# Kernel tuning notes

Measured on AMD Instinct MI355X. Metric: run time of the kernel, lower is better.

## Reference

```python
import jax, jax.numpy as jnp
import numpy as np

DIM = 1024
HEADS = 16
HEAD_DIM = DIM // HEADS  # 64


def get_rope_matrix(seq_len: int, dim: int) -> jnp.ndarray:
    # rope[s, d] = concat(cos(s * inv_freq), sin(s * inv_freq))  -> (seq_len, dim)
    half = dim // 2
    inv_freq = 1.0 / (10000.0 ** (jnp.arange(half, dtype=jnp.float32) / half))
    sinusoid = jnp.arange(seq_len, dtype=jnp.float32)[:, None] * inv_freq[None, :]
    return jnp.concatenate([jnp.cos(sinusoid), jnp.sin(sinusoid)], axis=-1)


def setup_inputs() -> dict:
    key = jax.random.key(0)
    ks = jax.random.split(key, 6)
    B, T, D = 2, 2048, DIM
    scale = 1.0 / np.sqrt(D)
    return {
        "x": jax.random.normal(ks[0], (B, T, D), dtype=jnp.float32),
        "Wq": jax.random.normal(ks[1], (D, D), dtype=jnp.float32) * scale,
        "Wk": jax.random.normal(ks[2], (D, D), dtype=jnp.float32) * scale,
        "Wv": jax.random.normal(ks[3], (D, D), dtype=jnp.float32) * scale,
        "Wo": jax.random.normal(ks[4], (D, D), dtype=jnp.float32) * scale,
        "bo": jax.random.normal(ks[5], (D,), dtype=jnp.float32) * 0.01,
    }


def reference(x, Wq, Wk, Wv, Wo, bo):
    B, T, D = x.shape
    H, hd = HEADS, HEAD_DIM

    # projections -> (B, H, T, hd)
    def split_heads(y):
        return y.reshape(B, T, H, hd).transpose(0, 2, 1, 3)

    q = split_heads(x @ Wq)
    k = split_heads(x @ Wk)
    v = split_heads(x @ Wv)

    rope = get_rope_matrix(T, hd)  # (T, hd)

    # apply_rope(v, rope): einsum('...nd,sd->...ns') contracts head_dim -> (B,H,T,T)
    v_r = jnp.einsum('bhnd,sd->bhns', v, rope)

    scores = jax.nn.softmax(jnp.einsum('bhnd,bhmd->bhnm', q, k) / jnp.sqrt(jnp.float32(hd)), axis=-1)
    out = jnp.einsum('bhnm,bhms->bhns', scores, v_r)  # (B,H,T,T)

    # apply_rope(out, rope.T): out2[...,n,s] = sum_t out[...,n,t] * rope[t,s] -> (B,H,T,hd)
    out = jnp.einsum('bhnt,ts->bhns', out, rope)

    out = out.transpose(0, 2, 1, 3).reshape(B, T, D)
    return out @ Wo + bo
```

## Files before the change

kernel.cpp:

```cpp
#include <hip/hip_runtime.h>
#include <math.h>

#define DIM 1024
#define NH 16
#define HD 64
#define TT 2048
#define NTOK 4096

typedef __bf16 bf8v __attribute__((ext_vector_type(8)));
typedef float f4v __attribute__((ext_vector_type(4)));
typedef float f16v __attribute__((ext_vector_type(16)));
typedef unsigned short us8 __attribute__((ext_vector_type(8)));
typedef unsigned short us4 __attribute__((ext_vector_type(4)));
typedef unsigned int u4v __attribute__((ext_vector_type(4)));

static __device__ __forceinline__ unsigned short f2bf(float f) {
    unsigned int u = __float_as_uint(f);
    u += 0x7FFFu + ((u >> 16) & 1u);
    return (unsigned short)(u >> 16);
}
static __device__ __forceinline__ bf8v ld8(const unsigned short* p) {
    return __builtin_bit_cast(bf8v, *(const us8*)p);
}
static __device__ __forceinline__ void gl_lds(const unsigned short* g, unsigned short* l) {
    __builtin_amdgcn_global_load_lds((const __attribute__((address_space(1))) unsigned int*)(g),
                                     (__attribute__((address_space(3))) unsigned int*)(l), 16, 0, 0);
}

__global__ void k_prep(const float* __restrict__ x, unsigned short* __restrict__ xb,
                       const float* __restrict__ Wq, const float* __restrict__ Wk,
                       const float* __restrict__ Wv, unsigned short* __restrict__ wt,
                       float* __restrict__ rope) {
    int tid = threadIdx.x;
    int bb = blockIdx.x;
    if (bb < 4096) {
        int i = bb * 256 + tid;
        float4 v = ((const float4*)x)[i];
        us4 o;
        o[0] = f2bf(v.x); o[1] = f2bf(v.y); o[2] = f2bf(v.z); o[3] = f2bf(v.w);
        *(us4*)&xb[i * 4] = o;
    } else if (bb < 7168) {
        __shared__ float tile[32][33];
        bb -= 4096;
        int z = bb >> 10, rem = bb & 1023;
        int bx = rem & 31, by = rem >> 5;
        const float* W = (z == 0) ? Wq : ((z == 1) ? Wk : Wv);
        int tx = tid & 31, ty = tid >> 5;
        int c0 = bx * 32, k0 = by * 32;
#pragma unroll
        for (int j = 0; j < 4; j++)
            tile[ty + j * 8][tx] = W[(k0 + ty + j * 8) * DIM + c0 + tx];
        __syncthreads();
        unsigned short* out = wt + z * DIM * DIM;
#pragma unroll
        for (int j = 0; j < 4; j++)
            out[(c0 + ty + j * 8) * DIM + k0 + tx] = f2bf(tile[tx][ty + j * 8]);
    } else {
        int i = (bb - 7168) * 256 + tid;
        int s = i >> 6, d = i & 63;
        float inv = exp2f(-(float)(d & 31) * (13.287712379549449f / 32.0f));
        float a = (float)s * inv;
        rope[i] = (d < 32) ? cosf(a) : sinf(a);
    }
}

__global__ void k_R(const float* __restrict__ rope, float* __restrict__ R) {
    __shared__ float red[256];
    int d = blockIdx.x;
    int e = threadIdx.x & 63, sl = threadIdx.x >> 6;
    const float* rp = rope + sl * 512 * 64;
    float acc = 0.f;
    for (int s = 0; s < 512; s++)
        acc += rp[s * 64 + d] * rp[s * 64 + e];
    red[threadIdx.x] = acc;
    __syncthreads();
    if (sl == 0)
        R[d * 64 + e] = (red[e] + red[e + 64]) + (red[e + 128] + red[e + 192]);
}

__global__ void k_wo2(const float* __restrict__ Wo, const float* __restrict__ R,
                      unsigned short* __restrict__ wo2t) {
    __shared__ float Ws[64 * 65];
    __shared__ float Rt[64 * 65];
    int tid = threadIdx.x;
    int h = blockIdx.y, j0 = blockIdx.x * 64;
    for (int idx = tid; idx < 4096; idx += 256) {
        int e = idx >> 6, j = idx & 63;
        Ws[e * 65 + j] = Wo[(h * 64 + e) * DIM + j0 + j];
        Rt[e * 65 + j] = R[j * 64 + e];
    }
    __syncthreads();
    int d = tid & 63, jb = (tid >> 6) * 16;
    float acc[16] = {};
    for (int e = 0; e < 64; e++) {
        float r = Rt[e * 65 + d];
#pragma unroll
        for (int jj = 0; jj < 16; jj++)
            acc[jj] += r * Ws[e * 65 + jb + jj];
    }
#pragma unroll
    for (int jj = 0; jj < 16; jj++)
        wo2t[(j0 + jb + jj) * DIM + h * 64 + d] = f2bf(acc[jj]);
}


__global__ __launch_bounds__(256, 3) void k_gemm_qkv(const unsigned short* __restrict__ A,
                                                     const unsigned short* __restrict__ Bt,
                                                     unsigned short* __restrict__ qk,
                                                     unsigned short* __restrict__ vt) {
    __shared__ unsigned short As[128 * 32];
    __shared__ unsigned short Bs[128 * 32];
    const int K = 1024;
    int tid = threadIdx.x;
    int lane = tid & 63, w = tid >> 6;
    int quad = lane >> 4, l16 = lane & 15;
    int m0 = blockIdx.y * 128, n0 = blockIdx.x * 128;
    int wm = (w >> 1) * 64, wn = (w & 1) * 64;

    int s0 = tid, s1 = 256 + tid;
    int r0 = s0 >> 2, cc0 = ((s0 & 3) ^ (r0 & 3)) * 8;
    int r1 = s1 >> 2, cc1 = ((s1 & 3) ^ (r1 & 3)) * 8;
    const unsigned short* Ag0 = A + (m0 + r0) * K + cc0;
    const unsigned short* Ag1 = A + (m0 + r1) * K + cc1;
    const unsigned short* Bg0 = Bt + (n0 + r0) * K + cc0;
    const unsigned short* Bg1 = Bt + (n0 + r1) * K + cc1;
    int qx = quad ^ (l16 & 3);

    f4v acc[4][4] = {};
    for (int k0 = 0; k0 < K; k0 += 32) {
        __syncthreads();
        gl_lds(Ag0 + k0, &As[s0 * 8]);
        gl_lds(Ag1 + k0, &As[s1 * 8]);
        gl_lds(Bg0 + k0, &Bs[s0 * 8]);
        gl_lds(Bg1 + k0, &Bs[s1 * 8]);
        __syncthreads();
        bf8v af[4], bf[4];
#pragma unroll
        for (int mt = 0; mt < 4; mt++)
            af[mt] = ld8(&As[(wm + mt * 16 + l16) * 32 + qx * 8]);
#pragma unroll
        for (int nt = 0; nt < 4; nt++)
            bf[nt] = ld8(&Bs[(wn + nt * 16 + l16) * 32 + qx * 8]);
#pragma unroll
        for (int mt = 0; mt < 4; mt++)
#pragma unroll
            for (int nt = 0; nt < 4; nt++)
                acc[mt][nt] = __builtin_amdgcn_mfma_f32_16x16x32_bf16(af[mt], bf[nt], acc[mt][nt], 0, 0, 0);
    }
#pragma unroll
    for (int mt = 0; mt < 4; mt++) {
#pragma unroll
        for (int nt = 0; nt < 4; nt++) {
            int gc = n0 + wn + nt * 16 + l16;
            int h = (gc >> 6) & 15;
            int d = gc & 63;
            if (gc < 2048) {
                float qs = (gc < 1024) ? 0.18033688011111793f : 1.0f;
                int mtx = gc >> 10;
                unsigned short* base = qk + mtx * (NTOK * DIM);
#pragma unroll
                for (int r = 0; r < 4; r++) {
                    int gm = m0 + wm + mt * 16 + quad * 4 + r;
                    int b = gm >> 11, t = gm & 2047;
                    base[((b * NH + h) * TT + t) * HD + d] = f2bf(acc[mt][nt][r] * qs);
                }
            } else {
                int gm0 = m0 + wm + mt * 16 + quad * 4;
                int b = gm0 >> 11, t = gm0 & 2047;
                us4 ov;
#pragma unroll
                for (int r = 0; r < 4; r++)
                    ov[r] = f2bf(acc[mt][nt][r]);
                *(us4*)&vt[(((b * NH + h) * HD) + d) * TT + t] = ov;
            }
        }
    }
}

__global__ __launch_bounds__(256, 3) void k_gemm_out(const unsigned short* __restrict__ Op,
                                                     const float* __restrict__ Ls,
                                                     const unsigned short* __restrict__ Bt,
                                                     const float* __restrict__ bo,
                                                     float* __restrict__ out) {
    __shared__ unsigned short As[128 * 32];
    __shared__ unsigned short Bs[128 * 32];
    const int K = 1024;
    int tid = threadIdx.x;
    int lane = tid & 63, w = tid >> 6;
    int quad = lane >> 4, l16 = lane & 15;
    int m0 = blockIdx.y * 128, n0 = blockIdx.x * 128;
    int wm = (w >> 1) * 64, wn = (w & 1) * 64;

    int s0 = tid, s1 = 256 + tid;
    int r0 = s0 >> 2, cc0 = ((s0 & 3) ^ (r0 & 3)) * 8;
    int r1 = s1 >> 2, cc1 = ((s1 & 3) ^ (r1 & 3)) * 8;
    int gm0 = m0 + r0, gm1 = m0 + r1;
    const unsigned short* Ag0 = Op + gm0 * K + cc0;
    const unsigned short* Ag1 = Op + gm1 * K + cc1;
    const unsigned short* Bg0 = Bt + (n0 + r0) * K + cc0;
    const unsigned short* Bg1 = Bt + (n0 + r1) * K + cc1;
    const float* L0 = Ls + (gm0 >> 11) * 16 * 2048 + (gm0 & 2047);
    const float* L1 = Ls + (gm1 >> 11) * 16 * 2048 + (gm1 & 2047);
    int qx = quad ^ (l16 & 3);

    us8 pa0 = *(const us8*)(Ag0);
    us8 pc0 = *(const us8*)(Ag0 + NTOK * DIM);
    us8 pa1 = *(const us8*)(Ag1);
    us8 pc1 = *(const us8*)(Ag1 + NTOK * DIM);
    float pl00 = L0[0], pl01 = L0[65536];
    float pl10 = L1[0], pl11 = L1[65536];

    f4v acc[4][4] = {};
    for (int k0 = 0; k0 < K; k0 += 32) {
        __syncthreads();
        gl_lds(Bg0 + k0, &Bs[s0 * 8]);
        gl_lds(Bg1 + k0, &Bs[s1 * 8]);
        {
            float inv0 = __builtin_amdgcn_rcpf(pl00 + pl01);
            float inv1 = __builtin_amdgcn_rcpf(pl10 + pl11);
            u4v o0, o1;
#pragma unroll
            for (int p = 0; p < 4; p++) {
                float va = (__uint_as_float((unsigned int)pa0[2 * p] << 16) +
                            __uint_as_float((unsigned int)pc0[2 * p] << 16)) * inv0;
                float vb = (__uint_as_float((unsigned int)pa0[2 * p + 1] << 16) +
                            __uint_as_float((unsigned int)pc0[2 * p + 1] << 16)) * inv0;
                unsigned int wd;
                asm("v_cvt_pk_bf16_f32 %0, %1, %2" : "=v"(wd) : "v"(va), "v"(vb));
                o0[p] = wd;
                float vc = (__uint_as_float((unsigned int)pa1[2 * p] << 16) +
                            __uint_as_float((unsigned int)pc1[2 * p] << 16)) * inv1;
                float vd = (__uint_as_float((unsigned int)pa1[2 * p + 1] << 16) +
                            __uint_as_float((unsigned int)pc1[2 * p + 1] << 16)) * inv1;
                asm("v_cvt_pk_bf16_f32 %0, %1, %2" : "=v"(wd) : "v"(vc), "v"(vd));
                o1[p] = wd;
            }
            *(u4v*)&As[s0 * 8] = o0;
            *(u4v*)&As[s1 * 8] = o1;
        }
        __syncthreads();
        {
            int kn = (k0 + 32) & 1023;
            int h0n = (kn + cc0) >> 6, h1n = (kn + cc1) >> 6;
            pa0 = *(const us8*)(Ag0 + kn);
            pc0 = *(const us8*)(Ag0 + NTOK * DIM + kn);
            pa1 = *(const us8*)(Ag1 + kn);
            pc1 = *(const us8*)(Ag1 + NTOK * DIM + kn);
            pl00 = L0[h0n * 2048]; pl01 = L0[65536 + h0n * 2048];
            pl10 = L1[h1n * 2048]; pl11 = L1[65536 + h1n * 2048];
        }
        bf8v af[4], bf[4];
#pragma unroll
        for (int mt = 0; mt < 4; mt++)
            af[mt] = ld8(&As[(wm + mt * 16 + l16) * 32 + qx * 8]);
#pragma unroll
        for (int nt = 0; nt < 4; nt++)
            bf[nt] = ld8(&Bs[(wn + nt * 16 + l16) * 32 + qx * 8]);
#pragma unroll
        for (int mt = 0; mt < 4; mt++)
#pragma unroll
            for (int nt = 0; nt < 4; nt++)
                acc[mt][nt] = __builtin_amdgcn_mfma_f32_16x16x32_bf16(af[mt], bf[nt], acc[mt][nt], 0, 0, 0);
    }
#pragma unroll
    for (int mt = 0; mt < 4; mt++) {
#pragma unroll
        for (int nt = 0; nt < 4; nt++) {
            int gc = n0 + wn + nt * 16 + l16;
            float bias = bo[gc];
#pragma unroll
            for (int r = 0; r < 4; r++) {
                int gm = m0 + wm + mt * 16 + quad * 4 + r;
                out[gm * DIM + gc] = acc[mt][nt][r] + bias;
            }
        }
    }
}

__global__ __launch_bounds__(256, 4) void k_flash(const unsigned short* __restrict__ qk,
                                                  const unsigned short* __restrict__ vt,
                                                  unsigned short* __restrict__ Op,
                                                  float* __restrict__ Ls) {
    __shared__ unsigned short Ks[2][64 * 64];
    __shared__ unsigned short Vs[2][64 * 64];
    int tid = threadIdx.x;
    int lane = tid & 63, w = tid >> 6;
    int q31 = lane & 31, hi = lane >> 5;
    int bid = blockIdx.x;
    int xcd = bid & 7, sl = bid >> 3;
    int bh = xcd * 4 + (sl & 3);
    int qt = (sl >> 2) & 15;
    int sp = sl >> 6;

    const unsigned short* Qg = qk + bh * (TT * HD);
    const unsigned short* Kg = qk + NTOK * DIM + bh * (TT * HD) + sp * 1024 * HD;
    const unsigned short* Vg = vt + bh * (HD * TT) + sp * 1024;

    int qrow = qt * 128 + w * 32 + q31;
    bf8v qf[4];
#pragma unroll
    for (int ks = 0; ks < 4; ks++)
        qf[ks] = ld8(Qg + qrow * HD + ks * 16 + hi * 8);

    int r0 = tid >> 3, sw = (tid & 7) ^ (r0 & 7);
    int offK0 = r0 * HD + sw * 8, offK1 = offK0 + 32 * HD;
    int offV0 = r0 * TT + sw * 8, offV1 = offV0 + 32 * TT;
    int dst0 = tid * 8, dst1 = dst0 + 2048;

#define STAGE(tile, bufsel) do {                                  \
        const unsigned short* kb_ = Kg + (tile) * 64 * HD;        \
        const unsigned short* vb_ = Vg + (tile) * 64;             \
        gl_lds(kb_ + offK0, &Ks[bufsel][dst0]);                   \
        gl_lds(kb_ + offK1, &Ks[bufsel][dst1]);                   \
        gl_lds(vb_ + offV0, &Vs[bufsel][dst0]);                   \
        gl_lds(vb_ + offV1, &Vs[bufsel][dst1]);                   \
    } while (0)

    STAGE(0, 0);
    STAGE(1, 1);

    f16v oacc[2] = {};
    float lsg = 0.f;
    int xsw = q31 & 7;

    for (int it = 0; it < 16; it++) {
        int cur = it & 1;
        if (it == 15) { asm volatile("s_waitcnt vmcnt(0)" ::: "memory"); }
        else          { asm volatile("s_waitcnt vmcnt(4)" ::: "memory"); }
        __builtin_amdgcn_s_barrier();
        asm volatile("" ::: "memory");

        const unsigned short* Kb = Ks[cur];
        const unsigned short* Vb = Vs[cur];

        bf8v kf0[4], kf1[4];
#pragma unroll
        for (int ks = 0; ks < 4; ks++) {
            kf0[ks] = ld8(&Kb[(q31) * 64 + ((2 * ks + hi) ^ xsw) * 8]);
            kf1[ks] = ld8(&Kb[(32 + q31) * 64 + ((2 * ks + hi) ^ xsw) * 8]);
        }
        f16v s0 = {}, s1 = {};
#pragma unroll
        for (int ks = 0; ks < 4; ks++) {
            s0 = __builtin_amdgcn_mfma_f32_32x32x16_bf16(kf0[ks], qf[ks], s0, 0, 0, 0);
            s1 = __builtin_amdgcn_mfma_f32_32x32x16_bf16(kf1[ks], qf[ks], s1, 0, 0, 0);
        }

        bf8v vf[2][4];
#pragma unroll
        for (int kk = 0; kk < 4; kk++) {
            vf[0][kk] = ld8(&Vb[(q31) * 64 + ((2 * kk + hi) ^ xsw) * 8]);
            vf[1][kk] = ld8(&Vb[(32 + q31) * 64 + ((2 * kk + hi) ^ xsw) * 8]);
        }

#pragma unroll
        for (int mt = 0; mt < 2; mt++) {
#pragma unroll
            for (int sub = 0; sub < 2; sub++) {
                const f16v& s = mt ? s1 : s0;
                float pe[8];
#pragma unroll
                for (int j = 0; j < 8; j++)
                    pe[j] = __builtin_amdgcn_exp2f(s[sub * 8 + j]);
                float t01 = pe[0] + pe[1], t23 = pe[2] + pe[3];
                float t45 = pe[4] + pe[5], t67 = pe[6] + pe[7];
                lsg += (t01 + t23) + (t45 + t67);
                unsigned int e0, e1, e2, e3;
                asm("v_cvt_pk_bf16_f32 %0, %1, %2" : "=v"(e0) : "v"(pe[0]), "v"(pe[1]));
                asm("v_cvt_pk_bf16_f32 %0, %1, %2" : "=v"(e1) : "v"(pe[2]), "v"(pe[3]));
                asm("v_cvt_pk_bf16_f32 %0, %1, %2" : "=v"(e2) : "v"(pe[4]), "v"(pe[5]));
                asm("v_cvt_pk_bf16_f32 %0, %1, %2" : "=v"(e3) : "v"(pe[6]), "v"(pe[7]));
                asm("v_permlane32_swap_b32 %0, %1" : "+v"(e0), "+v"(e2));
                asm("v_permlane32_swap_b32 %0, %1" : "+v"(e1), "+v"(e3));
                u4v pv = {e0, e1, e2, e3};
                bf8v pb = __builtin_bit_cast(bf8v, pv);
                int kk = mt * 2 + sub;
                oacc[0] = __builtin_amdgcn_mfma_f32_32x32x16_bf16(vf[0][kk], pb, oacc[0], 0, 0, 0);
                oacc[1] = __builtin_amdgcn_mfma_f32_32x32x16_bf16(vf[1][kk], pb, oacc[1], 0, 0, 0);
            }
        }

        __builtin_amdgcn_s_barrier();
        asm volatile("" ::: "memory");
        if (it < 14) STAGE(it + 2, cur);
    }
#undef STAGE

    float lsum = lsg + __shfl_xor(lsg, 32, 64);
    int b = bh >> 4, h = bh & 15;
    unsigned short* dst = Op + sp * (NTOK * DIM) + ((b * TT) + qrow) * DIM + h * HD + hi * 4;
#pragma unroll
    for (int mtd = 0; mtd < 2; mtd++) {
#pragma unroll
        for (int g4 = 0; g4 < 4; g4++) {
            us4 ov;
#pragma unroll
            for (int r = 0; r < 4; r++)
                ov[r] = f2bf(oacc[mtd][g4 * 4 + r]);
            *(us4*)&dst[mtd * 32 + g4 * 8] = ov;
        }
    }
    if (hi == 0)
        Ls[sp * 65536 + bh * 2048 + qrow] = lsum;
}

extern "C" void kernel_launch(void* const* d_in, const int* in_sizes, int n_in,
                              void* d_out, int out_size, void* d_ws, size_t ws_size,
                              hipStream_t stream) {
    const float* x  = (const float*)d_in[0];
    const float* Wq = (const float*)d_in[1];
    const float* Wk = (const float*)d_in[2];
    const float* Wv = (const float*)d_in[3];
    const float* Wo = (const float*)d_in[4];
    const float* bo = (const float*)d_in[5];
    float* out = (float*)d_out;
    char* ws = (char*)d_ws;

    unsigned short* Xb    = (unsigned short*)(ws);
    unsigned short* Wqkvt = (unsigned short*)(ws + 8388608);
    unsigned short* Op    = (unsigned short*)(ws);
    unsigned short* QK    = (unsigned short*)(ws + 16777216);
    unsigned short* Vt    = (unsigned short*)(ws + 33554432);
    unsigned short* Wo2t  = (unsigned short*)(ws + 50331648);
    float*          rope  = (float*)(ws + 52428800);
    float*          Rm    = (float*)(ws + 52953088);
    float*          Ls    = (float*)(ws + 52969472);

    hipLaunchKernelGGL(k_prep,     dim3(7680),   dim3(256), 0, stream, x, Xb, Wq, Wk, Wv, Wqkvt, rope);
    hipLaunchKernelGGL(k_R,        dim3(64),     dim3(256), 0, stream, rope, Rm);
    hipLaunchKernelGGL(k_wo2,      dim3(16, 16), dim3(256), 0, stream, Wo, Rm, Wo2t);
    hipLaunchKernelGGL(k_gemm_qkv, dim3(24, 32), dim3(256), 0, stream, Xb, Wqkvt, QK, Vt);
    hipLaunchKernelGGL(k_flash,    dim3(1024),   dim3(256), 0, stream, QK, Vt, Op, Ls);
    hipLaunchKernelGGL(k_gemm_out, dim3(8, 32),  dim3(256), 0, stream, Op, Ls, Wo2t, bo, out);
}
```

Baseline: 229.3 us.

## Split rope Gram reduction across blocks and retile output GEMM for more blocks

The R = rope^T rope reduction was done by 64 blocks, each looping over 512 rows. It is now split across 512 blocks that each sum 64 rows and combine partial sums with atomicAdd into an Rm buffer zeroed in k_prep. The output GEMM moves from 128x128 tiles (256 blocks) to 64x128 tiles (512 blocks) with an XCD-aware block-to-tile mapping and a smaller accumulator per wave. Both changes aim to fill more CUs on these small kernels. In exchange they add atomics, nondeterministic summation order, and less reuse of each loaded tile in the GEMM.

```diff
diff --git a/kernel.cpp b/kernel.cpp
--- a/kernel.cpp
+++ b/kernel.cpp
@@ -30,7 +30,7 @@
 __global__ void k_prep(const float* __restrict__ x, unsigned short* __restrict__ xb,
                        const float* __restrict__ Wq, const float* __restrict__ Wk,
                        const float* __restrict__ Wv, unsigned short* __restrict__ wt,
-                       float* __restrict__ rope) {
+                       float* __restrict__ rope, float* __restrict__ Rm) {
     int tid = threadIdx.x;
     int bb = blockIdx.x;
     if (bb < 4096) {
@@ -55,27 +55,29 @@
 #pragma unroll
         for (int j = 0; j < 4; j++)
             out[(c0 + ty + j * 8) * DIM + k0 + tx] = f2bf(tile[tx][ty + j * 8]);
-    } else {
+    } else if (bb < 7680) {
         int i = (bb - 7168) * 256 + tid;
         int s = i >> 6, d = i & 63;
         float inv = exp2f(-(float)(d & 31) * (13.287712379549449f / 32.0f));
         float a = (float)s * inv;
         rope[i] = (d < 32) ? cosf(a) : sinf(a);
+    } else {
+        Rm[(bb - 7680) * 256 + tid] = 0.f;
     }
 }
 
 __global__ void k_R(const float* __restrict__ rope, float* __restrict__ R) {
     __shared__ float red[256];
-    int d = blockIdx.x;
+    int d = blockIdx.x & 63, sg = blockIdx.x >> 6;
     int e = threadIdx.x & 63, sl = threadIdx.x >> 6;
-    const float* rp = rope + sl * 512 * 64;
+    const float* rp = rope + (sg * 256 + sl * 64) * 64;
     float acc = 0.f;
-    for (int s = 0; s < 512; s++)
+    for (int s = 0; s < 64; s++)
         acc += rp[s * 64 + d] * rp[s * 64 + e];
     red[threadIdx.x] = acc;
     __syncthreads();
     if (sl == 0)
-        R[d * 64 + e] = (red[e] + red[e + 64]) + (red[e + 128] + red[e + 192]);
+        atomicAdd(&R[d * 64 + e], (red[e] + red[e + 64]) + (red[e + 128] + red[e + 192]));
 }
 
 __global__ void k_wo2(const float* __restrict__ Wo, const float* __restrict__ R,
@@ -177,48 +179,44 @@
     }
 }
 
-__global__ __launch_bounds__(256, 3) void k_gemm_out(const unsigned short* __restrict__ Op,
+__global__ __launch_bounds__(256, 2) void k_gemm_out(const unsigned short* __restrict__ Op,
                                                      const float* __restrict__ Ls,
                                                      const unsigned short* __restrict__ Bt,
                                                      const float* __restrict__ bo,
                                                      float* __restrict__ out) {
-    __shared__ unsigned short As[128 * 32];
+    __shared__ unsigned short As[64 * 32];
     __shared__ unsigned short Bs[128 * 32];
     const int K = 1024;
     int tid = threadIdx.x;
     int lane = tid & 63, w = tid >> 6;
     int quad = lane >> 4, l16 = lane & 15;
-    int m0 = blockIdx.y * 128, n0 = blockIdx.x * 128;
-    int wm = (w >> 1) * 64, wn = (w & 1) * 64;
-
-    int s0 = tid, s1 = 256 + tid;
-    int r0 = s0 >> 2, cc0 = ((s0 & 3) ^ (r0 & 3)) * 8;
-    int r1 = s1 >> 2, cc1 = ((s1 & 3) ^ (r1 & 3)) * 8;
-    int gm0 = m0 + r0, gm1 = m0 + r1;
-    const unsigned short* Ag0 = Op + gm0 * K + cc0;
-    const unsigned short* Ag1 = Op + gm1 * K + cc1;
-    const unsigned short* Bg0 = Bt + (n0 + r0) * K + cc0;
-    const unsigned short* Bg1 = Bt + (n0 + r1) * K + cc1;
+    int bid = blockIdx.x;
+    int xcd = bid & 7, slot = bid >> 3;
+    int y = xcd * 8 + (slot & 7);
+    int x = slot >> 3;
+    int m0 = y * 64, n0 = x * 128;
+    int wn = w * 32;
+
+    int rr = tid >> 2, cc = ((tid & 3) ^ (rr & 3)) * 8;
+    int gm0 = m0 + rr;
+    const unsigned short* Ag0 = Op + gm0 * K + cc;
+    const unsigned short* Bg0 = Bt + (n0 + rr) * K + cc;
+    const unsigned short* Bg1 = Bt + (n0 + 64 + rr) * K + cc;
     const float* L0 = Ls + (gm0 >> 11) * 16 * 2048 + (gm0 & 2047);
-    const float* L1 = Ls + (gm1 >> 11) * 16 * 2048 + (gm1 & 2047);
     int qx = quad ^ (l16 & 3);
 
     us8 pa0 = *(const us8*)(Ag0);
     us8 pc0 = *(const us8*)(Ag0 + NTOK * DIM);
-    us8 pa1 = *(const us8*)(Ag1);
-    us8 pc1 = *(const us8*)(Ag1 + NTOK * DIM);
     float pl00 = L0[0], pl01 = L0[65536];
-    float pl10 = L1[0], pl11 = L1[65536];
-
-    f4v acc[4][4] = {};
+
+    f4v acc[4][2] = {};
     for (int k0 = 0; k0 < K; k0 += 32) {
         __syncthreads();
-        gl_lds(Bg0 + k0, &Bs[s0 * 8]);
-        gl_lds(Bg1 + k0, &Bs[s1 * 8]);
+        gl_lds(Bg0 + k0, &Bs[tid * 8]);
+        gl_lds(Bg1 + k0, &Bs[(256 + tid) * 8]);
         {
             float inv0 = __builtin_amdgcn_rcpf(pl00 + pl01);
-            float inv1 = __builtin_amdgcn_rcpf(pl10 + pl11);
-            u4v o0, o1;
+            u4v o0;
 #pragma unroll
             for (int p = 0; p < 4; p++) {
                 float va = (__uint_as_float((unsigned int)pa0[2 * p] << 16) +
@@ -228,49 +226,39 @@
                 unsigned int wd;
                 asm("v_cvt_pk_bf16_f32 %0, %1, %2" : "=v"(wd) : "v"(va), "v"(vb));
                 o0[p] = wd;
-                float vc = (__uint_as_float((unsigned int)pa1[2 * p] << 16) +
-                            __uint_as_float((unsigned int)pc1[2 * p] << 16)) * inv1;
-                float vd = (__uint_as_float((unsigned int)pa1[2 * p + 1] << 16) +
-                            __uint_as_float((unsigned int)pc1[2 * p + 1] << 16)) * inv1;
-                asm("v_cvt_pk_bf16_f32 %0, %1, %2" : "=v"(wd) : "v"(vc), "v"(vd));
-                o1[p] = wd;
             }
-            *(u4v*)&As[s0 * 8] = o0;
-            *(u4v*)&As[s1 * 8] = o1;
+            *(u4v*)&As[tid * 8] = o0;
         }
         __syncthreads();
         {
             int kn = (k0 + 32) & 1023;
-            int h0n = (kn + cc0) >> 6, h1n = (kn + cc1) >> 6;
+            int hn = (kn + cc) >> 6;
             pa0 = *(const us8*)(Ag0 + kn);
             pc0 = *(const us8*)(Ag0 + NTOK * DIM + kn);
-            pa1 = *(const us8*)(Ag1 + kn);
-            pc1 = *(const us8*)(Ag1 + NTOK * DIM + kn);
-            pl00 = L0[h0n * 2048]; pl01 = L0[65536 + h0n * 2048];
-            pl10 = L1[h1n * 2048]; pl11 = L1[65536 + h1n * 2048];
-        }
-        bf8v af[4], bf[4];
+            pl00 = L0[hn * 2048]; pl01 = L0[65536 + hn * 2048];
+        }
+        bf8v af[4], bf[2];
 #pragma unroll
         for (int mt = 0; mt < 4; mt++)
-            af[mt] = ld8(&As[(wm + mt * 16 + l16) * 32 + qx * 8]);
-#pragma unroll
-        for (int nt = 0; nt < 4; nt++)
+            af[mt] = ld8(&As[(mt * 16 + l16) * 32 + qx * 8]);
+#pragma unroll
+        for (int nt = 0; nt < 2; nt++)
             bf[nt] = ld8(&Bs[(wn + nt * 16 + l16) * 32 + qx * 8]);
 #pragma unroll
         for (int mt = 0; mt < 4; mt++)
 #pragma unroll
-            for (int nt = 0; nt < 4; nt++)
+            for (int nt = 0; nt < 2; nt++)
                 acc[mt][nt] = __builtin_amdgcn_mfma_f32_16x16x32_bf16(af[mt], bf[nt], acc[mt][nt], 0, 0, 0);
     }
 #pragma unroll
     for (int mt = 0; mt < 4; mt++) {
 #pragma unroll
-        for (int nt = 0; nt < 4; nt++) {
+        for (int nt = 0; nt < 2; nt++) {
             int gc = n0 + wn + nt * 16 + l16;
             float bias = bo[gc];
 #pragma unroll
             for (int r = 0; r < 4; r++) {
-                int gm = m0 + wm + mt * 16 + quad * 4 + r;
+                int gm = m0 + mt * 16 + quad * 4 + r;
                 out[gm * DIM + gc] = acc[mt][nt][r] + bias;
             }
         }
@@ -426,10 +414,10 @@
     float*          Rm    = (float*)(ws + 52953088);
     float*          Ls    = (float*)(ws + 52969472);
 
-    hipLaunchKernelGGL(k_prep,     dim3(7680),   dim3(256), 0, stream, x, Xb, Wq, Wk, Wv, Wqkvt, rope);
-    hipLaunchKernelGGL(k_R,        dim3(64),     dim3(256), 0, stream, rope, Rm);
+    hipLaunchKernelGGL(k_prep,     dim3(7696),   dim3(256), 0, stream, x, Xb, Wq, Wk, Wv, Wqkvt, rope, Rm);
+    hipLaunchKernelGGL(k_R,        dim3(512),    dim3(256), 0, stream, rope, Rm);
     hipLaunchKernelGGL(k_wo2,      dim3(16, 16), dim3(256), 0, stream, Wo, Rm, Wo2t);
     hipLaunchKernelGGL(k_gemm_qkv, dim3(24, 32), dim3(256), 0, stream, Xb, Wqkvt, QK, Vt);
     hipLaunchKernelGGL(k_flash,    dim3(1024),   dim3(256), 0, stream, QK, Vt, Op, Ls);
-    hipLaunchKernelGGL(k_gemm_out, dim3(8, 32),  dim3(256), 0, stream, Op, Ls, Wo2t, bo, out);
-}
+    hipLaunchKernelGGL(k_gemm_out, dim3(512),    dim3(256), 0, stream, Op, Ls, Wo2t, bo, out);
+}
```

Result: faster. 202.8 us (-11.5%).
